# Kernel optimization log

Measured on AMD Instinct MI355X. Metric: run time of the kernel, lower is better.

Reference implementation:

```python
import jax, jax.numpy as jnp
import numpy as np

B, S, D = 2, 2048, 1024
H, DH = 16, 64
DM = 4096
NEG = 1e10


def setup_inputs() -> dict:
    key = jax.random.key(0)
    ks = jax.random.split(key, 8)
    sc = 1.0 / np.sqrt(D)
    return {
        "x": jax.random.normal(ks[0], (B, S, D), jnp.float32),
        "W_Q": jax.random.normal(ks[1], (H, DH, D), jnp.float32) * sc,
        "W_K": jax.random.normal(ks[2], (H, DH, D), jnp.float32) * sc,
        "W_V": jax.random.normal(ks[3], (H, DH, D), jnp.float32) * sc,
        "W_O": jax.random.normal(ks[4], (D, H * DH), jnp.float32) * sc,
        "W_in": jax.random.normal(ks[5], (DM, D), jnp.float32) * sc,
        "b_in": jnp.zeros((DM,), jnp.float32),
        "W_out": jax.random.normal(ks[6], (D, DM), jnp.float32) * sc,
        "b_out": jnp.zeros((D,), jnp.float32),
    }


def reference(x, W_Q, W_K, W_V, W_O, W_in, b_in, W_out, b_out):
    b, s, d = x.shape
    d_head = W_Q.shape[1]
    # --- Attention (faithful to original einsum/mask formulation) ---
    q = jnp.einsum('ihd,bpd->biph', W_Q, x)
    k = jnp.einsum('ihd,bpd->biph', W_K, x)
    v = jnp.einsum('ihd,bpd->biph', W_V, x)
    scores = jnp.einsum('biph,biqh->biqp', k, q)  # [b,i,q,p]
    # original: t.tril(scores) - 1e10 * (1 - triu(ones)) ; mask buffer is triu
    triu = jnp.triu(jnp.ones((s, s), x.dtype))
    masked = jnp.tril(scores) - NEG * (1.0 - triu)
    attn = jax.nn.softmax(masked / np.sqrt(d_head), axis=-1)
    z = jnp.einsum('biph,biqp->biqh', v, attn)          # [b,i,q,h]
    z_flat = z.transpose(0, 2, 1, 3).reshape(b, s, -1)   # b q (i h)
    attn_out = jnp.einsum('df,bqf->bqd', W_O, z_flat)
    # --- Block residual structure (as written: x = attn(x); x = x + x) ---
    mid = attn_out + attn_out
    # --- MLP ---
    pre = jnp.einsum('md,bpd->bpm', W_in, mid) + b_in
    h = jax.nn.relu(pre)
    mlp_out = jnp.einsum('dm,bpm->bpd', W_out, h) + b_out
    return mid + mlp_out
```

## Files before the change

### kernel.cpp

```cpp
#include <hip/hip_runtime.h>
#include <hip/hip_bf16.h>
#include <stdint.h>

typedef unsigned short ushort_t;
typedef __attribute__((ext_vector_type(8))) short short8;
typedef __attribute__((ext_vector_type(4))) float floatx4;

#define DEV __device__ __forceinline__

DEV ushort_t f2b(float f) {
  uint32_t x = __float_as_uint(f);
  uint32_t r = (x + 0x7FFFu + ((x >> 16) & 1u)) >> 16;
  return (ushort_t)r;
}
DEV float b2f(ushort_t u) { return __uint_as_float(((uint32_t)u) << 16); }

DEV void async16(const ushort_t* g, ushort_t* l) {
  __builtin_amdgcn_global_load_lds(
      (const __attribute__((address_space(1))) void*)g,
      (__attribute__((address_space(3))) void*)l, 16, 0, 0);
}

struct Cvt7 {
  const float* src[7];
  ushort_t* dst[7];
  unsigned start[8];
};
__global__ void cvt_all(Cvt7 a) {
  unsigned idx = blockIdx.x * blockDim.x + threadIdx.x;
  if (idx >= a.start[7]) return;
  int seg = 0;
#pragma unroll
  for (int j = 1; j < 7; j++) seg += (idx >= a.start[j]) ? 1 : 0;
  unsigned off = idx - a.start[seg];
  float4 v = ((const float4*)a.src[seg])[off];
  ((ushort4*)a.dst[seg])[off] = make_ushort4(f2b(v.x), f2b(v.y), f2b(v.z), f2b(v.w));
}

template <int MODE>
__launch_bounds__(256)
__global__ void gemm_bt(const ushort_t* __restrict__ A, const ushort_t* __restrict__ Bm,
                        int M, int N, int K, int Ksplit,
                        ushort_t* __restrict__ outB, float* __restrict__ outF,
                        const float* __restrict__ bias) {
  __shared__ alignas(16) ushort_t As[128 * 32];
  __shared__ alignas(16) ushort_t Bs[128 * 32];
  const int tid = threadIdx.x;
  const int wave = tid >> 6, lane = tid & 63;
  const int wm = wave >> 1, wn = wave & 1;
  const int m0 = blockIdx.y * 128, n0 = blockIdx.x * 128;
  const int kz = blockIdx.z * Ksplit;

  floatx4 acc[4][4];
#pragma unroll
  for (int i = 0; i < 4; i++)
#pragma unroll
    for (int j = 0; j < 4; j++) acc[i][j] = (floatx4){0.f, 0.f, 0.f, 0.f};

  const int srow = wave * 32 + (lane >> 2);
  const int scol = (((lane & 3) ^ ((lane >> 3) & 3)) * 8);
  const ushort_t* gA0 = A + (size_t)(m0 + srow) * K + kz + scol;
  const ushort_t* gA1 = gA0 + (size_t)16 * K;
  const ushort_t* gB0 = Bm + (size_t)(n0 + srow) * K + kz + scol;
  const ushort_t* gB1 = gB0 + (size_t)16 * K;
  ushort_t* lA0 = As + wave * 1024;
  ushort_t* lA1 = As + wave * 1024 + 512;
  ushort_t* lB0 = Bs + wave * 1024;
  ushort_t* lB1 = Bs + wave * 1024 + 512;

  const int fr = lane & 15, fq = lane >> 4;
  const int cb = fq ^ ((fr >> 1) & 3);
  const ushort_t* rdA = As + (wm * 64 + fr) * 32 + cb * 8;
  const ushort_t* rdB = Bs + (wn * 64 + fr) * 32 + cb * 8;

  for (int k0 = 0; k0 < Ksplit; k0 += 32) {
    async16(gA0, lA0);
    async16(gA1, lA1);
    async16(gB0, lB0);
    async16(gB1, lB1);
    gA0 += 32; gA1 += 32; gB0 += 32; gB1 += 32;
    __syncthreads();
    short8 af[4], bfv[4];
#pragma unroll
    for (int mt = 0; mt < 4; mt++) af[mt] = *(const short8*)(rdA + mt * 16 * 32);
#pragma unroll
    for (int nt = 0; nt < 4; nt++) bfv[nt] = *(const short8*)(rdB + nt * 16 * 32);
#pragma unroll
    for (int mt = 0; mt < 4; mt++)
#pragma unroll
      for (int nt = 0; nt < 4; nt++)
        acc[mt][nt] = __builtin_amdgcn_mfma_f32_16x16x32_bf16(af[mt], bfv[nt], acc[mt][nt], 0, 0, 0);
    __syncthreads();
  }

  const int crow = m0 + wm * 64 + (lane >> 4) * 4;
  const int ccol = n0 + wn * 64 + (lane & 15);
  const size_t zoff = (size_t)blockIdx.z * M * N;
#pragma unroll
  for (int mt = 0; mt < 4; mt++)
#pragma unroll
    for (int nt = 0; nt < 4; nt++) {
      floatx4 a = acc[mt][nt];
#pragma unroll
      for (int r = 0; r < 4; r++) {
        const int gm = crow + mt * 16 + r;
        const int gn = ccol + nt * 16;
        const size_t idx = (size_t)gm * N + gn;
        float v = a[r];
        if constexpr (MODE == 0) {
          outB[idx] = f2b(v);
        } else if constexpr (MODE == 1) {
          float t = 2.f * v;
          outB[idx] = f2b(t);
          outF[idx] = t + bias[gn];
        } else if constexpr (MODE == 2) {
          float t = v + bias[gn];
          outB[idx] = f2b(t > 0.f ? t : 0.f);
        } else {
          outF[zoff + idx] = v;
        }
      }
    }
}

__launch_bounds__(256)
__global__ void reduce4(const float4* __restrict__ P, float4* __restrict__ out, int n4) {
  int i = blockIdx.x * blockDim.x + threadIdx.x;
  int st = gridDim.x * blockDim.x;
  for (; i < n4; i += st) {
    float4 a = out[i];
    float4 p0 = P[i], p1 = P[i + 1048576], p2 = P[i + 2097152], p3 = P[i + 3145728];
    a.x += p0.x + p1.x + p2.x + p3.x;
    a.y += p0.y + p1.y + p2.y + p3.y;
    a.z += p0.z + p1.z + p2.z + p3.z;
    a.w += p0.w + p1.w + p2.w + p3.w;
    out[i] = a;
  }
}

__launch_bounds__(256)
__global__ void attn1(const ushort_t* __restrict__ qkv,
                      float* __restrict__ eG, float* __restrict__ psumG) {
  const int c = blockIdx.x & 31;
  const int i = (blockIdx.x >> 5) & 15;
  const int b = blockIdx.x >> 9;
  const int t = threadIdx.x, wave = t >> 6, h = t & 63;
  const size_t rowbase = (size_t)b * 2048 * 3072;
  float vacc = 0.f;
#pragma unroll 4
  for (int r = 0; r < 16; r++) {
    const int s = c * 64 + wave * 16 + r;
    const size_t rb = rowbase + (size_t)s * 3072 + i * 64 + h;
    float q = b2f(qkv[rb]);
    float k = b2f(qkv[rb + 1024]);
    float v = b2f(qkv[rb + 2048]);
    float d = q * k;
#pragma unroll
    for (int off = 32; off > 0; off >>= 1) d += __shfl_xor(d, off, 64);
    if (h == 0) eG[((size_t)(b * 16 + i)) * 2048 + s] = __expf(d * 0.125f);
    vacc += v;
  }
  __shared__ float vs[4][64];
  vs[wave][h] = vacc;
  __syncthreads();
  if (t < 64)
    psumG[(((size_t)(b * 16 + i)) * 32 + c) * 64 + t] =
        vs[0][t] + vs[1][t] + vs[2][t] + vs[3][t];
}

__launch_bounds__(256)
__global__ void attn2(const ushort_t* __restrict__ qkv,
                      const float* __restrict__ eG, const float* __restrict__ psumG,
                      ushort_t* __restrict__ Z) {
  const int wave = threadIdx.x >> 6, h = threadIdx.x & 63;
  const int c = (blockIdx.x & 7) * 4 + wave;
  const int i = (blockIdx.x >> 3) & 15;
  const int b = blockIdx.x >> 7;
  const size_t rowbase = (size_t)b * 2048 * 3072;
  const size_t pbase = ((size_t)(b * 16 + i)) * 32;
  float run = 0.f;
#pragma unroll 8
  for (int cc = c + 1; cc < 32; cc++) run += psumG[(pbase + cc) * 64 + h];
  const size_t ebase = ((size_t)(b * 16 + i)) * 2048;
  for (int t4 = 3; t4 >= 0; t4--) {
    float vv[16], ee[16];
#pragma unroll
    for (int j = 0; j < 16; j++) {
      const int s = c * 64 + t4 * 16 + j;
      vv[j] = b2f(qkv[rowbase + (size_t)s * 3072 + 2048 + i * 64 + h]);
      ee[j] = eG[ebase + s];
    }
#pragma unroll
    for (int j = 15; j >= 0; j--) {
      const int s = c * 64 + t4 * 16 + j;
      float z = (ee[j] * vv[j] + run) / (ee[j] + (float)(2047 - s));
      Z[((size_t)b * 2048 + s) * 1024 + i * 64 + h] = f2b(z);
      run += vv[j];
    }
  }
}

extern "C" void kernel_launch(void* const* d_in, const int* in_sizes, int n_in,
                              void* d_out, int out_size, void* d_ws, size_t ws_size,
                              hipStream_t stream) {
  const float* x     = (const float*)d_in[0];
  const float* W_Q   = (const float*)d_in[1];
  const float* W_K   = (const float*)d_in[2];
  const float* W_V   = (const float*)d_in[3];
  const float* W_O   = (const float*)d_in[4];
  const float* W_in  = (const float*)d_in[5];
  const float* b_in  = (const float*)d_in[6];
  const float* W_out = (const float*)d_in[7];
  const float* b_out = (const float*)d_in[8];
  float* out = (float*)d_out;

  char* base = (char*)d_ws;
  const size_t MB = 1048576;
  ushort_t* Xb    = (ushort_t*)(base + 0 * MB);
  ushort_t* Wqkv  = (ushort_t*)(base + 8 * MB);
  ushort_t* WOb   = (ushort_t*)(base + 14 * MB);
  ushort_t* Z     = (ushort_t*)(base + 16 * MB);
  ushort_t* QKV   = (ushort_t*)(base + 24 * MB);
  ushort_t* midb  = (ushort_t*)(base + 48 * MB);
  ushort_t* Winb  = (ushort_t*)(base + 56 * MB);
  float*    P     = (float*)(base + 0 * MB);
  ushort_t* Woutb = (ushort_t*)(base + 64 * MB);
  ushort_t* Hb    = (ushort_t*)(base + 72 * MB);
  float*    eG    = (float*)(base + 104 * MB);
  float*    psumG = (float*)(base + 104 * MB + 262144);

  Cvt7 ca;
  ca.src[0] = x;     ca.dst[0] = Xb;
  ca.src[1] = W_Q;   ca.dst[1] = Wqkv;
  ca.src[2] = W_K;   ca.dst[2] = Wqkv + 1048576;
  ca.src[3] = W_V;   ca.dst[3] = Wqkv + 2097152;
  ca.src[4] = W_O;   ca.dst[4] = WOb;
  ca.src[5] = W_in;  ca.dst[5] = Winb;
  ca.src[6] = W_out; ca.dst[6] = Woutb;
  unsigned n4s[7] = {1048576, 262144, 262144, 262144, 262144, 1048576, 1048576};
  unsigned acc4 = 0;
  for (int j = 0; j < 7; j++) { ca.start[j] = acc4; acc4 += n4s[j]; }
  ca.start[7] = acc4;
  cvt_all<<<dim3((acc4 + 255) / 256), dim3(256), 0, stream>>>(ca);

  gemm_bt<0><<<dim3(24, 32), 256, 0, stream>>>(Xb, Wqkv, 4096, 3072, 1024, 1024,
                                               QKV, nullptr, nullptr);
  attn1<<<dim3(1024), 256, 0, stream>>>(QKV, eG, psumG);
  attn2<<<dim3(256), 256, 0, stream>>>(QKV, eG, psumG, Z);
  gemm_bt<1><<<dim3(8, 32), 256, 0, stream>>>(Z, WOb, 4096, 1024, 1024, 1024,
                                              midb, out, b_out);
  gemm_bt<2><<<dim3(32, 32), 256, 0, stream>>>(midb, Winb, 4096, 4096, 1024, 1024,
                                               Hb, nullptr, b_in);
  gemm_bt<3><<<dim3(8, 32, 4), 256, 0, stream>>>(Hb, Woutb, 4096, 1024, 4096, 1024,
                                                 nullptr, P, nullptr);
  reduce4<<<dim3(1024), 256, 0, stream>>>((const float4*)P, (float4*)out, 1048576);
}
```

Baseline: 340.2 us.

## Double GEMM K-tile to 64 and drop split-K with separate reduction

Each GEMM iteration now stages a 128x64 K-slab per operand, using a new 8-way XOR swizzle, and issues two MFMA rounds per barrier pair. This halves the number of synchronisation points per K. The final MLP GEMM no longer uses 4-way split-K with a partial buffer and a reduce kernel. It accumulates directly into the output, which removes one launch and the 64MB partial write/read. The cost is that the final GEMM now runs only 256 blocks over K=4096, which lowers parallelism, and LDS use doubles per block.

```diff
diff --git a/kernel.cpp b/kernel.cpp
--- a/kernel.cpp
+++ b/kernel.cpp
@@ -40,16 +40,15 @@
 template <int MODE>
 __launch_bounds__(256)
 __global__ void gemm_bt(const ushort_t* __restrict__ A, const ushort_t* __restrict__ Bm,
-                        int M, int N, int K, int Ksplit,
+                        int M, int N, int K,
                         ushort_t* __restrict__ outB, float* __restrict__ outF,
                         const float* __restrict__ bias) {
-  __shared__ alignas(16) ushort_t As[128 * 32];
-  __shared__ alignas(16) ushort_t Bs[128 * 32];
+  __shared__ alignas(16) ushort_t As[128 * 64];
+  __shared__ alignas(16) ushort_t Bs[128 * 64];
   const int tid = threadIdx.x;
   const int wave = tid >> 6, lane = tid & 63;
   const int wm = wave >> 1, wn = wave & 1;
   const int m0 = blockIdx.y * 128, n0 = blockIdx.x * 128;
-  const int kz = blockIdx.z * Ksplit;
 
   floatx4 acc[4][4];
 #pragma unroll
@@ -57,45 +56,45 @@
 #pragma unroll
     for (int j = 0; j < 4; j++) acc[i][j] = (floatx4){0.f, 0.f, 0.f, 0.f};
 
-  const int srow = wave * 32 + (lane >> 2);
-  const int scol = (((lane & 3) ^ ((lane >> 3) & 3)) * 8);
-  const ushort_t* gA0 = A + (size_t)(m0 + srow) * K + kz + scol;
-  const ushort_t* gA1 = gA0 + (size_t)16 * K;
-  const ushort_t* gB0 = Bm + (size_t)(n0 + srow) * K + kz + scol;
-  const ushort_t* gB1 = gB0 + (size_t)16 * K;
-  ushort_t* lA0 = As + wave * 1024;
-  ushort_t* lA1 = As + wave * 1024 + 512;
-  ushort_t* lB0 = Bs + wave * 1024;
-  ushort_t* lB1 = Bs + wave * 1024 + 512;
+  const int srow = wave * 32 + (lane >> 3);
+  const int scol = (((lane & 7) ^ ((lane >> 3) & 7)) * 8);
+  const ushort_t* gA = A + (size_t)(m0 + srow) * K + scol;
+  const ushort_t* gB = Bm + (size_t)(n0 + srow) * K + scol;
+  ushort_t* lA = As + wave * 2048;
+  ushort_t* lB = Bs + wave * 2048;
 
   const int fr = lane & 15, fq = lane >> 4;
-  const int cb = fq ^ ((fr >> 1) & 3);
-  const ushort_t* rdA = As + (wm * 64 + fr) * 32 + cb * 8;
-  const ushort_t* rdB = Bs + (wn * 64 + fr) * 32 + cb * 8;
-
-  for (int k0 = 0; k0 < Ksplit; k0 += 32) {
-    async16(gA0, lA0);
-    async16(gA1, lA1);
-    async16(gB0, lB0);
-    async16(gB1, lB1);
-    gA0 += 32; gA1 += 32; gB0 += 32; gB1 += 32;
+  const ushort_t* rdA = As + (wm * 64 + fr) * 64;
+  const ushort_t* rdB = Bs + (wn * 64 + fr) * 64;
+  const int sw = fr & 7;
+
+  for (int k0 = 0; k0 < K; k0 += 64) {
+#pragma unroll
+    for (int j = 0; j < 4; j++) {
+      async16(gA + (size_t)j * 8 * K, lA + j * 512);
+      async16(gB + (size_t)j * 8 * K, lB + j * 512);
+    }
+    gA += 64; gB += 64;
     __syncthreads();
-    short8 af[4], bfv[4];
-#pragma unroll
-    for (int mt = 0; mt < 4; mt++) af[mt] = *(const short8*)(rdA + mt * 16 * 32);
-#pragma unroll
-    for (int nt = 0; nt < 4; nt++) bfv[nt] = *(const short8*)(rdB + nt * 16 * 32);
-#pragma unroll
-    for (int mt = 0; mt < 4; mt++)
-#pragma unroll
-      for (int nt = 0; nt < 4; nt++)
-        acc[mt][nt] = __builtin_amdgcn_mfma_f32_16x16x32_bf16(af[mt], bfv[nt], acc[mt][nt], 0, 0, 0);
+#pragma unroll
+    for (int h = 0; h < 2; h++) {
+      const int co = ((h * 4 + fq) ^ sw) * 8;
+      short8 af[4], bfv[4];
+#pragma unroll
+      for (int mt = 0; mt < 4; mt++) af[mt] = *(const short8*)(rdA + mt * 16 * 64 + co);
+#pragma unroll
+      for (int nt = 0; nt < 4; nt++) bfv[nt] = *(const short8*)(rdB + nt * 16 * 64 + co);
+#pragma unroll
+      for (int mt = 0; mt < 4; mt++)
+#pragma unroll
+        for (int nt = 0; nt < 4; nt++)
+          acc[mt][nt] = __builtin_amdgcn_mfma_f32_16x16x32_bf16(af[mt], bfv[nt], acc[mt][nt], 0, 0, 0);
+    }
     __syncthreads();
   }
 
   const int crow = m0 + wm * 64 + (lane >> 4) * 4;
   const int ccol = n0 + wn * 64 + (lane & 15);
-  const size_t zoff = (size_t)blockIdx.z * M * N;
 #pragma unroll
   for (int mt = 0; mt < 4; mt++)
 #pragma unroll
@@ -117,25 +116,10 @@
           float t = v + bias[gn];
           outB[idx] = f2b(t > 0.f ? t : 0.f);
         } else {
-          outF[zoff + idx] = v;
+          outF[idx] += v;
         }
       }
     }
-}
-
-__launch_bounds__(256)
-__global__ void reduce4(const float4* __restrict__ P, float4* __restrict__ out, int n4) {
-  int i = blockIdx.x * blockDim.x + threadIdx.x;
-  int st = gridDim.x * blockDim.x;
-  for (; i < n4; i += st) {
-    float4 a = out[i];
-    float4 p0 = P[i], p1 = P[i + 1048576], p2 = P[i + 2097152], p3 = P[i + 3145728];
-    a.x += p0.x + p1.x + p2.x + p3.x;
-    a.y += p0.y + p1.y + p2.y + p3.y;
-    a.z += p0.z + p1.z + p2.z + p3.z;
-    a.w += p0.w + p1.w + p2.w + p3.w;
-    out[i] = a;
-  }
 }
 
 __launch_bounds__(256)
@@ -223,7 +207,6 @@
   ushort_t* QKV   = (ushort_t*)(base + 24 * MB);
   ushort_t* midb  = (ushort_t*)(base + 48 * MB);
   ushort_t* Winb  = (ushort_t*)(base + 56 * MB);
-  float*    P     = (float*)(base + 0 * MB);
   ushort_t* Woutb = (ushort_t*)(base + 64 * MB);
   ushort_t* Hb    = (ushort_t*)(base + 72 * MB);
   float*    eG    = (float*)(base + 104 * MB);
@@ -243,15 +226,14 @@
   ca.start[7] = acc4;
   cvt_all<<<dim3((acc4 + 255) / 256), dim3(256), 0, stream>>>(ca);
 
-  gemm_bt<0><<<dim3(24, 32), 256, 0, stream>>>(Xb, Wqkv, 4096, 3072, 1024, 1024,
+  gemm_bt<0><<<dim3(24, 32), 256, 0, stream>>>(Xb, Wqkv, 4096, 3072, 1024,
                                                QKV, nullptr, nullptr);
   attn1<<<dim3(1024), 256, 0, stream>>>(QKV, eG, psumG);
   attn2<<<dim3(256), 256, 0, stream>>>(QKV, eG, psumG, Z);
-  gemm_bt<1><<<dim3(8, 32), 256, 0, stream>>>(Z, WOb, 4096, 1024, 1024, 1024,
+  gemm_bt<1><<<dim3(8, 32), 256, 0, stream>>>(Z, WOb, 4096, 1024, 1024,
                                               midb, out, b_out);
-  gemm_bt<2><<<dim3(32, 32), 256, 0, stream>>>(midb, Winb, 4096, 4096, 1024, 1024,
+  gemm_bt<2><<<dim3(32, 32), 256, 0, stream>>>(midb, Winb, 4096, 4096, 1024,
                                                Hb, nullptr, b_in);
-  gemm_bt<3><<<dim3(8, 32, 4), 256, 0, stream>>>(Hb, Woutb, 4096, 1024, 4096, 1024,
-                                                 nullptr, P, nullptr);
-  reduce4<<<dim3(1024), 256, 0, stream>>>((const float4*)P, (float4*)out, 1048576);
-}
+  gemm_bt<3><<<dim3(8, 32), 256, 0, stream>>>(Hb, Woutb, 4096, 1024, 4096,
+                                              nullptr, out, b_out);
+}
```

Result: faster. 327.5 us (-3.7%).
